# Kernel tuning notes

Measured on AMD Instinct MI355X. Metric: run time of the kernel, lower is better.

The kernel has to match this reference:

```python
import jax, jax.numpy as jnp
import numpy as np
import math

D_MODEL = 1024
D_HEAD = 64
BATCH = 8
SEQ = 2048


def setup_inputs() -> dict:
    key = jax.random.key(0)
    ks = jax.random.split(key, 5)
    s = 0.02
    return {
        "residual_stream": jax.random.normal(ks[0], (BATCH, SEQ, D_MODEL), dtype=jnp.float32),
        "Wq": jax.random.normal(ks[1], (D_HEAD, D_MODEL), dtype=jnp.float32) * s,
        "Wk": jax.random.normal(ks[2], (D_HEAD, D_MODEL), dtype=jnp.float32) * s,
        "Wv": jax.random.normal(ks[3], (D_HEAD, D_MODEL), dtype=jnp.float32) * s,
        "Wo": jax.random.normal(ks[4], (D_MODEL, D_HEAD), dtype=jnp.float32) * s,
    }


def reference(residual_stream, Wq, Wk, Wv, Wo):
    # NOTE: module scales by 1/sqrt(d_model), NOT 1/sqrt(d_head)
    scale = 1.0 / math.sqrt(D_MODEL)
    q = jnp.einsum('bsd,hd->bsh', residual_stream, Wq)  # [B,S,Dh]
    k = jnp.einsum('bsd,hd->bsh', residual_stream, Wk)  # [B,S,Dh]
    scores = jnp.einsum('bqh,bkh->bqk', q, k) * scale   # [B,S,S]
    seq = scores.shape[-1]
    causal = jnp.tril(jnp.ones((seq, seq), dtype=bool))
    scores = jnp.where(causal[None, :, :], scores, jnp.float32(-jnp.inf))
    attn = jax.nn.softmax(scores, axis=-1)
    # O applied to V *before* the attention-weighted sum (as in the module)
    x = jnp.einsum('bsh,dh->bsd', jnp.einsum('bsd,hd->bsh', residual_stream, Wv), Wo)  # [B,S,Dm]
    return jnp.einsum('bqk,bkd->bqd', attn, x)
```

## Files before the change

kernel.cpp:

```cpp
#include <hip/hip_runtime.h>

#define SEQ 2048
#define DMODEL 1024
#define DHEAD 64
#define NROWS 16384
#define ATT_SCALE 0.03125f

typedef __attribute__((ext_vector_type(8))) short bf16x8;
typedef __attribute__((ext_vector_type(4))) float f32x4;
typedef __attribute__((ext_vector_type(4))) unsigned int u32x4;
typedef __attribute__((ext_vector_type(4))) unsigned short u16x4;
typedef __attribute__((ext_vector_type(4))) float fl4;

#define MFMA16(a,b,c) __builtin_amdgcn_mfma_f32_16x16x32_bf16((a),(b),(c),0,0,0)
#define GLL16(g, l) __builtin_amdgcn_global_load_lds( \
    (const __attribute__((address_space(1))) void*)(g), \
    (__attribute__((address_space(3))) void*)(l), 16, 0, 0)

__device__ __forceinline__ unsigned short f2bf(float f) {
    union { float f; unsigned int u; } v; v.f = f;
    unsigned int u = v.u;
    unsigned int r = u + 0x7fffu + ((u >> 16) & 1u);
    return (unsigned short)(r >> 16);
}

__global__ __launch_bounds__(256) void k_cvt(
    const float* __restrict__ Wq, const float* __restrict__ Wk,
    const float* __restrict__ Wv, const float* __restrict__ Wo,
    unsigned short* __restrict__ Wb,
    unsigned short* __restrict__ Wob)
{
    int i4 = blockIdx.x * 256 + threadIdx.x;
    const int W1 = 16384;
    const float* src; unsigned short* dst; int off;
    if (i4 < 3 * W1) {
        int which = i4 / W1;
        off = i4 - which * W1;
        src = (which == 0) ? Wq : (which == 1) ? Wk : Wv;
        dst = Wb + (size_t)which * 65536;
    } else {
        off = i4 - 3 * W1; src = Wo; dst = Wob;
    }
    fl4 v = reinterpret_cast<const fl4*>(src)[off];
    u16x4 o;
    o[0] = f2bf(v[0]); o[1] = f2bf(v[1]); o[2] = f2bf(v[2]); o[3] = f2bf(v[3]);
    reinterpret_cast<u16x4*>(dst)[off] = o;
}

__global__ __launch_bounds__(256) void k_qkv(
    const float* __restrict__ x,
    const unsigned short* __restrict__ Wb,
    unsigned short* __restrict__ Qb,
    unsigned short* __restrict__ Kb,
    unsigned short* __restrict__ Vt)
{
    __shared__ __align__(16) char smem[81920];

    int tid = threadIdx.x;
    int wave = tid >> 6, lane = tid & 63, g = lane >> 4, lr = lane & 15;
    int mbase = blockIdx.x * 64;

    const float* xsrc[4];
#pragma unroll
    for (int j = 0; j < 4; ++j) {
        int ci = (wave * 4 + j) * 64 + lane;
        int row = ci >> 4, c = ci & 15, cg = c ^ (row & 7);
        xsrc[j] = x + (size_t)(mbase + row) * DMODEL + cg * 4;
    }
    const unsigned short* wsrc[6];
#pragma unroll
    for (int j = 0; j < 6; ++j) {
        int ci = (wave * 6 + j) * 64 + lane;
        int row = ci >> 3, c = ci & 7, cg = c ^ (row & 7);
        wsrc[j] = Wb + (size_t)row * DMODEL + cg * 8;
    }

    f32x4 acc[12];
#pragma unroll
    for (int f = 0; f < 12; ++f) acc[f] = (f32x4){0.f, 0.f, 0.f, 0.f};

#pragma unroll
    for (int j = 0; j < 4; ++j) GLL16(xsrc[j], smem + (wave * 4 + j) * 1024);
#pragma unroll
    for (int j = 0; j < 6; ++j) GLL16(wsrc[j], smem + 32768 + (wave * 6 + j) * 1024);

    for (int ks = 0; ks < 16; ++ks) {
        int cur = ks & 1;
        if (ks < 15) {
            int nb = cur ^ 1;
#pragma unroll
            for (int j = 0; j < 4; ++j)
                GLL16(xsrc[j] + (ks + 1) * 64, smem + nb * 16384 + (wave * 4 + j) * 1024);
#pragma unroll
            for (int j = 0; j < 6; ++j)
                GLL16(wsrc[j] + (ks + 1) * 64, smem + 32768 + nb * 24576 + (wave * 6 + j) * 1024);
            asm volatile("s_waitcnt vmcnt(10)" ::: "memory");
        } else {
            asm volatile("s_waitcnt vmcnt(0)" ::: "memory");
        }
        __builtin_amdgcn_s_barrier();
        asm volatile("" ::: "memory");

        const float* Xf = (const float*)(smem + cur * 16384);
        const unsigned short* Wf = (const unsigned short*)(smem + 32768 + cur * 24576);
        int arow = wave * 16 + lr;
#pragma unroll
        for (int kc = 0; kc < 2; ++kc) {
            int c0 = (kc * 8 + g * 2) ^ (lr & 7);
            int c1 = (kc * 8 + g * 2 + 1) ^ (lr & 7);
            fl4 xa = *(const fl4*)&Xf[arow * 64 + c0 * 4];
            fl4 xb = *(const fl4*)&Xf[arow * 64 + c1 * 4];
            bf16x8 a;
            a[0] = (short)f2bf(xa[0]); a[1] = (short)f2bf(xa[1]);
            a[2] = (short)f2bf(xa[2]); a[3] = (short)f2bf(xa[3]);
            a[4] = (short)f2bf(xb[0]); a[5] = (short)f2bf(xb[1]);
            a[6] = (short)f2bf(xb[2]); a[7] = (short)f2bf(xb[3]);
            __builtin_amdgcn_s_setprio(1);
#pragma unroll
            for (int f = 0; f < 12; ++f) {
                int brow = f * 16 + lr;
                int cb = (kc * 4 + g) ^ (lr & 7);
                bf16x8 b = *(const bf16x8*)&Wf[brow * 64 + cb * 8];
                acc[f] = MFMA16(a, b, acc[f]);
            }
            __builtin_amdgcn_s_setprio(0);
        }
        asm volatile("" ::: "memory");
        __builtin_amdgcn_s_barrier();
    }

    int mrow = mbase + wave * 16 + g * 4;
#pragma unroll
    for (int f = 0; f < 8; ++f) {
        int col = f * 16 + lr;
#pragma unroll
        for (int r = 0; r < 4; ++r) {
            unsigned short bv = f2bf(acc[f][r]);
            if (f < 4) Qb[(size_t)(mrow + r) * DHEAD + col] = bv;
            else       Kb[(size_t)(mrow + r) * DHEAD + col - 64] = bv;
        }
    }
    unsigned short* tmp = (unsigned short*)smem;
#pragma unroll
    for (int f = 8; f < 12; ++f) {
        int h = (f - 8) * 16 + lr;
#pragma unroll
        for (int r = 0; r < 4; ++r)
            tmp[(wave * 16 + g * 4 + r) * 72 + h] = f2bf(acc[f][r]);
    }
    __syncthreads();
    int b = mbase >> 11, sbase = mbase & 2047;
    int h = tid >> 2, sc = tid & 3;
    u32x4 o0, o1;
#pragma unroll
    for (int j = 0; j < 4; ++j) {
        o0[j] = (unsigned int)tmp[(sc * 16 + 2 * j) * 72 + h] |
                ((unsigned int)tmp[(sc * 16 + 2 * j + 1) * 72 + h] << 16);
        o1[j] = (unsigned int)tmp[(sc * 16 + 8 + 2 * j) * 72 + h] |
                ((unsigned int)tmp[(sc * 16 + 9 + 2 * j) * 72 + h] << 16);
    }
    size_t off = ((size_t)(b * 64 + h)) * SEQ + sbase + sc * 16;
    *reinterpret_cast<u32x4*>(&Vt[off]) = o0;
    *reinterpret_cast<u32x4*>(&Vt[off + 8]) = o1;
}

__global__ __launch_bounds__(128) void k_attn(
    const unsigned short* __restrict__ Qb,
    const unsigned short* __restrict__ Kb,
    const unsigned short* __restrict__ Vt,
    float* __restrict__ Op,
    float* __restrict__ Lp)
{
    __shared__ __align__(16) char smem[36864];

    int tid = threadIdx.x;
    int wave = tid >> 6, lane = tid & 63, g = lane >> 4, lr = lane & 15;
    int bid = blockIdx.x;
    int qt = 63 - (bid >> 4);
    int sub = bid & 15;
    int b = sub >> 1, chunk = sub & 1;
    int nt = qt / 2 + 1;
    int my_nt = (nt + 1 - chunk) >> 1;
    int qg = qt * 32 + wave * 16;
    size_t qrowbase = (size_t)(b * SEQ) + qg;

    bf16x8 aq[2];
#pragma unroll
    for (int kc = 0; kc < 2; ++kc)
        aq[kc] = *reinterpret_cast<const bf16x8*>(
            &Qb[(qrowbase + lr) * DHEAD + kc * 32 + g * 8]);

    const unsigned short* ksrc[4];
    const unsigned short* vsrc[4];
#pragma unroll
    for (int j = 0; j < 4; ++j) {
        int ci = wave * 256 + j * 64 + lane;
        int row = ci >> 3, c = ci & 7, cg = c ^ (row & 7);
        ksrc[j] = Kb + ((size_t)(b * SEQ) + row) * DHEAD + cg * 8;
        vsrc[j] = Vt + ((size_t)(b * DHEAD) + row) * SEQ + cg * 8;
    }

    float l_part[4];
    f32x4 of[4];
#pragma unroll
    for (int r = 0; r < 4; ++r) l_part[r] = 0.f;
#pragma unroll
    for (int f = 0; f < 4; ++f) of[f] = (f32x4){0.f, 0.f, 0.f, 0.f};

    if (my_nt > 0) {
#pragma unroll
        for (int j = 0; j < 4; ++j)
            GLL16(ksrc[j] + (size_t)chunk * 64 * DHEAD, smem + wave * 4096 + j * 1024);
#pragma unroll
        for (int j = 0; j < 4; ++j)
            GLL16(vsrc[j] + chunk * 64, smem + 16384 + wave * 4096 + j * 1024);

        for (int i = 0; i < my_nt; ++i) {
            int t = chunk + 2 * i;
            int cur = i & 1;
            if (i + 1 < my_nt) {
                int nb = cur ^ 1;
#pragma unroll
                for (int j = 0; j < 4; ++j)
                    GLL16(ksrc[j] + (size_t)(t + 2) * 64 * DHEAD,
                          smem + nb * 8192 + wave * 4096 + j * 1024);
#pragma unroll
                for (int j = 0; j < 4; ++j)
                    GLL16(vsrc[j] + (t + 2) * 64,
                          smem + 16384 + nb * 8192 + wave * 4096 + j * 1024);
                asm volatile("s_waitcnt vmcnt(8)" ::: "memory");
            } else {
                asm volatile("s_waitcnt vmcnt(0)" ::: "memory");
            }
            __builtin_amdgcn_s_barrier();
            asm volatile("" ::: "memory");

            const unsigned short* Kl = (const unsigned short*)(smem + cur * 8192);
            const unsigned short* Vl = (const unsigned short*)(smem + 16384 + cur * 8192);
            unsigned short* Pl = (unsigned short*)(smem + 32768) + wave * 1024;
            int kvb = t * 64;

            f32x4 s[4];
#pragma unroll
            for (int f = 0; f < 4; ++f) s[f] = (f32x4){0.f, 0.f, 0.f, 0.f};
            __builtin_amdgcn_s_setprio(1);
#pragma unroll
            for (int kc = 0; kc < 2; ++kc) {
#pragma unroll
                for (int f = 0; f < 4; ++f) {
                    int brow = f * 16 + lr;
                    int cb = (kc * 4 + g) ^ (lr & 7);
                    bf16x8 bk = *(const bf16x8*)&Kl[brow * 64 + cb * 8];
                    s[f] = MFMA16(aq[kc], bk, s[f]);
                }
            }
            __builtin_amdgcn_s_setprio(0);

#pragma unroll
            for (int f = 0; f < 4; ++f) {
                int kvg = kvb + f * 16 + lr;
#pragma unroll
                for (int r = 0; r < 4; ++r) {
                    int qr = qg + g * 4 + r;
                    float p = (kvg > qr) ? 0.f : __expf(s[f][r] * ATT_SCALE);
                    s[f][r] = p;
                    l_part[r] += p;
                }
            }
#pragma unroll
            for (int f = 0; f < 4; ++f) {
#pragma unroll
                for (int r = 0; r < 4; ++r) {
                    int row = g * 4 + r, col = f * 16 + lr;
                    int ch = (col >> 3) ^ (row & 7);
                    Pl[row * 64 + ch * 8 + (col & 7)] = f2bf(s[f][r]);
                }
            }
#pragma unroll
            for (int kc = 0; kc < 2; ++kc) {
                int cp = (kc * 4 + g) ^ (lr & 7);
                bf16x8 ap = *(const bf16x8*)&Pl[lr * 64 + cp * 8];
                __builtin_amdgcn_s_setprio(1);
#pragma unroll
                for (int fd = 0; fd < 4; ++fd) {
                    int vrow = fd * 16 + lr;
                    int cv = (kc * 4 + g) ^ (lr & 7);
                    bf16x8 bv = *(const bf16x8*)&Vl[vrow * 64 + cv * 8];
                    of[fd] = MFMA16(ap, bv, of[fd]);
                }
                __builtin_amdgcn_s_setprio(0);
            }
            asm volatile("" ::: "memory");
            __builtin_amdgcn_s_barrier();
        }
    }

    float* opb = Op + ((size_t)chunk * NROWS + qrowbase) * 64;
#pragma unroll
    for (int r = 0; r < 4; ++r) {
        float ls = l_part[r];
        ls += __shfl_xor(ls, 1); ls += __shfl_xor(ls, 2);
        ls += __shfl_xor(ls, 4); ls += __shfl_xor(ls, 8);
        if (lr == 0)
            Lp[(size_t)chunk * NROWS + qrowbase + g * 4 + r] = ls;
#pragma unroll
        for (int fd = 0; fd < 4; ++fd)
            opb[(g * 4 + r) * 64 + fd * 16 + lr] = of[fd][r];
    }
}

__global__ __launch_bounds__(256) void k_oproj(
    const float* __restrict__ Op,
    const float* __restrict__ Lp,
    const unsigned short* __restrict__ Wob,
    float* __restrict__ out)
{
    __shared__ __align__(16) unsigned short Wl[256 * 64];
    int tid = threadIdx.x;
    int wave = tid >> 6, lane = tid & 63, g = lane >> 4, lr = lane & 15;
    int mb = blockIdx.x * 64, nb = blockIdx.y * 256;

#pragma unroll
    for (int p = 0; p < 8; ++p) {
        int idx = p * 256 + tid;
        int row = idx >> 3, c = idx & 7;
        int ch = c ^ (row & 7);
        u32x4 v = *reinterpret_cast<const u32x4*>(
            &Wob[(size_t)(nb + row) * DHEAD + c * 8]);
        *reinterpret_cast<u32x4*>(&Wl[row * 64 + ch * 8]) = v;
    }
    __syncthreads();

    int row = mb + wave * 16 + lr;
    float inv = 1.0f / (Lp[row] + Lp[NROWS + row]);
    bf16x8 ao[2];
#pragma unroll
    for (int kc = 0; kc < 2; ++kc) {
        const float* p0 = &Op[(size_t)row * 64 + kc * 32 + g * 8];
        const float* p1 = &Op[(size_t)(NROWS + row) * 64 + kc * 32 + g * 8];
        fl4 a0 = *(const fl4*)p0, b0 = *(const fl4*)(p0 + 4);
        fl4 a1 = *(const fl4*)p1, b1 = *(const fl4*)(p1 + 4);
#pragma unroll
        for (int j = 0; j < 4; ++j) {
            ao[kc][j]     = (short)f2bf((a0[j] + a1[j]) * inv);
            ao[kc][j + 4] = (short)f2bf((b0[j] + b1[j]) * inv);
        }
    }

    f32x4 acc[16];
#pragma unroll
    for (int f = 0; f < 16; ++f) acc[f] = (f32x4){0.f, 0.f, 0.f, 0.f};
#pragma unroll
    for (int kc = 0; kc < 2; ++kc) {
        __builtin_amdgcn_s_setprio(1);
#pragma unroll
        for (int f = 0; f < 16; ++f) {
            int brow = f * 16 + lr;
            int cb = (kc * 4 + g) ^ (brow & 7);
            bf16x8 bw = *reinterpret_cast<const bf16x8*>(&Wl[brow * 64 + cb * 8]);
            acc[f] = MFMA16(ao[kc], bw, acc[f]);
        }
        __builtin_amdgcn_s_setprio(0);
    }
    int mrow = mb + wave * 16 + g * 4;
#pragma unroll
    for (int f = 0; f < 16; ++f) {
#pragma unroll
        for (int r = 0; r < 4; ++r)
            out[(size_t)(mrow + r) * DMODEL + nb + f * 16 + lr] = acc[f][r];
    }
}

extern "C" void kernel_launch(void* const* d_in, const int* in_sizes, int n_in,
                              void* d_out, int out_size, void* d_ws, size_t ws_size,
                              hipStream_t stream) {
    const float* x  = (const float*)d_in[0];
    const float* Wq = (const float*)d_in[1];
    const float* Wk = (const float*)d_in[2];
    const float* Wv = (const float*)d_in[3];
    const float* Wo = (const float*)d_in[4];
    float* out = (float*)d_out;

    unsigned short* Wb  = (unsigned short*)d_ws;
    unsigned short* Wob = Wb + 196608;
    unsigned short* Qb  = Wob + 65536;
    unsigned short* Kb  = Qb + 1048576;
    unsigned short* Vt  = Kb + 1048576;
    float* Op = (float*)(Vt + 1048576);
    float* Lp = Op + 2 * NROWS * 64;

    k_cvt<<<256, 256, 0, stream>>>(Wq, Wk, Wv, Wo, Wb, Wob);
    k_qkv<<<256, 256, 0, stream>>>(x, Wb, Qb, Kb, Vt);
    k_attn<<<1024, 128, 0, stream>>>(Qb, Kb, Vt, Op, Lp);
    k_oproj<<<dim3(256, 4), 256, 0, stream>>>(Op, Lp, Wob, out);
}
```

Baseline: 68.05 us.

## Enlarge attention query tiles, skip masked KV tiles, use packed bf16 conversion

The attention kernel now runs 4 waves per block over 64 query rows instead of 2 waves over 32. Each K/V tile loaded into shared memory is therefore reused by twice as many query rows, and the grid is halved. Waves whose rows lie entirely above a KV tile skip its compute, and fully unmasked tiles drop the mask test. The exp is rewritten as exp2 with a prescaled constant. Separately, fp32-to-bf16 packing in the QKV and output-projection kernels uses the hardware v_cvt_pk_bf16_f32 instruction instead of software rounding. The risk is wave divergence at the barriers and lower occupancy from the larger blocks.

```diff
diff --git a/kernel.cpp b/kernel.cpp
--- a/kernel.cpp
+++ b/kernel.cpp
@@ -4,7 +4,7 @@
 #define DMODEL 1024
 #define DHEAD 64
 #define NROWS 16384
-#define ATT_SCALE 0.03125f
+#define ATT_SC2 0.0450842300667f
 
 typedef __attribute__((ext_vector_type(8))) short bf16x8;
 typedef __attribute__((ext_vector_type(4))) float f32x4;
@@ -22,6 +22,12 @@
     unsigned int u = v.u;
     unsigned int r = u + 0x7fffu + ((u >> 16) & 1u);
     return (unsigned short)(r >> 16);
+}
+
+__device__ __forceinline__ unsigned int cvtpk(float lo, float hi) {
+    unsigned int d;
+    asm volatile("v_cvt_pk_bf16_f32 %0, %1, %2" : "=v"(d) : "v"(lo), "v"(hi));
+    return d;
 }
 
 __global__ __launch_bounds__(256) void k_cvt(
@@ -110,18 +116,16 @@
             int c1 = (kc * 8 + g * 2 + 1) ^ (lr & 7);
             fl4 xa = *(const fl4*)&Xf[arow * 64 + c0 * 4];
             fl4 xb = *(const fl4*)&Xf[arow * 64 + c1 * 4];
-            bf16x8 a;
-            a[0] = (short)f2bf(xa[0]); a[1] = (short)f2bf(xa[1]);
-            a[2] = (short)f2bf(xa[2]); a[3] = (short)f2bf(xa[3]);
-            a[4] = (short)f2bf(xb[0]); a[5] = (short)f2bf(xb[1]);
-            a[6] = (short)f2bf(xb[2]); a[7] = (short)f2bf(xb[3]);
+            union { unsigned int u[4]; bf16x8 v; } a;
+            a.u[0] = cvtpk(xa[0], xa[1]); a.u[1] = cvtpk(xa[2], xa[3]);
+            a.u[2] = cvtpk(xb[0], xb[1]); a.u[3] = cvtpk(xb[2], xb[3]);
             __builtin_amdgcn_s_setprio(1);
 #pragma unroll
             for (int f = 0; f < 12; ++f) {
                 int brow = f * 16 + lr;
                 int cb = (kc * 4 + g) ^ (lr & 7);
                 bf16x8 b = *(const bf16x8*)&Wf[brow * 64 + cb * 8];
-                acc[f] = MFMA16(a, b, acc[f]);
+                acc[f] = MFMA16(a.v, b, acc[f]);
             }
             __builtin_amdgcn_s_setprio(0);
         }
@@ -164,25 +168,25 @@
     *reinterpret_cast<u32x4*>(&Vt[off + 8]) = o1;
 }
 
-__global__ __launch_bounds__(128) void k_attn(
+__global__ __launch_bounds__(256) void k_attn(
     const unsigned short* __restrict__ Qb,
     const unsigned short* __restrict__ Kb,
     const unsigned short* __restrict__ Vt,
     float* __restrict__ Op,
     float* __restrict__ Lp)
 {
-    __shared__ __align__(16) char smem[36864];
+    __shared__ __align__(16) char smem[40960];
 
     int tid = threadIdx.x;
     int wave = tid >> 6, lane = tid & 63, g = lane >> 4, lr = lane & 15;
     int bid = blockIdx.x;
-    int qt = 63 - (bid >> 4);
+    int qt = 31 - (bid >> 4);
     int sub = bid & 15;
     int b = sub >> 1, chunk = sub & 1;
-    int nt = qt / 2 + 1;
+    int nt = qt + 1;
     int my_nt = (nt + 1 - chunk) >> 1;
-    int qg = qt * 32 + wave * 16;
-    size_t qrowbase = (size_t)(b * SEQ) + qg;
+    int qw = qt * 64 + wave * 16;
+    size_t qrowbase = (size_t)(b * SEQ) + qw;
 
     bf16x8 aq[2];
 #pragma unroll
@@ -190,11 +194,11 @@
         aq[kc] = *reinterpret_cast<const bf16x8*>(
             &Qb[(qrowbase + lr) * DHEAD + kc * 32 + g * 8]);
 
-    const unsigned short* ksrc[4];
-    const unsigned short* vsrc[4];
-#pragma unroll
-    for (int j = 0; j < 4; ++j) {
-        int ci = wave * 256 + j * 64 + lane;
+    const unsigned short* ksrc[2];
+    const unsigned short* vsrc[2];
+#pragma unroll
+    for (int j = 0; j < 2; ++j) {
+        int ci = j * 256 + tid;
         int row = ci >> 3, c = ci & 7, cg = c ^ (row & 7);
         ksrc[j] = Kb + ((size_t)(b * SEQ) + row) * DHEAD + cg * 8;
         vsrc[j] = Vt + ((size_t)(b * DHEAD) + row) * SEQ + cg * 8;
@@ -209,86 +213,100 @@
 
     if (my_nt > 0) {
 #pragma unroll
-        for (int j = 0; j < 4; ++j)
-            GLL16(ksrc[j] + (size_t)chunk * 64 * DHEAD, smem + wave * 4096 + j * 1024);
-#pragma unroll
-        for (int j = 0; j < 4; ++j)
-            GLL16(vsrc[j] + chunk * 64, smem + 16384 + wave * 4096 + j * 1024);
+        for (int j = 0; j < 2; ++j)
+            GLL16(ksrc[j] + (size_t)chunk * 64 * DHEAD, smem + j * 4096 + wave * 1024);
+#pragma unroll
+        for (int j = 0; j < 2; ++j)
+            GLL16(vsrc[j] + chunk * 64, smem + 16384 + j * 4096 + wave * 1024);
 
         for (int i = 0; i < my_nt; ++i) {
             int t = chunk + 2 * i;
             int cur = i & 1;
+            int kvb = t * 64;
             if (i + 1 < my_nt) {
                 int nb = cur ^ 1;
 #pragma unroll
-                for (int j = 0; j < 4; ++j)
+                for (int j = 0; j < 2; ++j)
                     GLL16(ksrc[j] + (size_t)(t + 2) * 64 * DHEAD,
-                          smem + nb * 8192 + wave * 4096 + j * 1024);
-#pragma unroll
-                for (int j = 0; j < 4; ++j)
+                          smem + nb * 8192 + j * 4096 + wave * 1024);
+#pragma unroll
+                for (int j = 0; j < 2; ++j)
                     GLL16(vsrc[j] + (t + 2) * 64,
-                          smem + 16384 + nb * 8192 + wave * 4096 + j * 1024);
-                asm volatile("s_waitcnt vmcnt(8)" ::: "memory");
+                          smem + 16384 + nb * 8192 + j * 4096 + wave * 1024);
+                asm volatile("s_waitcnt vmcnt(4)" ::: "memory");
             } else {
                 asm volatile("s_waitcnt vmcnt(0)" ::: "memory");
             }
             __builtin_amdgcn_s_barrier();
             asm volatile("" ::: "memory");
 
-            const unsigned short* Kl = (const unsigned short*)(smem + cur * 8192);
-            const unsigned short* Vl = (const unsigned short*)(smem + 16384 + cur * 8192);
-            unsigned short* Pl = (unsigned short*)(smem + 32768) + wave * 1024;
-            int kvb = t * 64;
-
-            f32x4 s[4];
-#pragma unroll
-            for (int f = 0; f < 4; ++f) s[f] = (f32x4){0.f, 0.f, 0.f, 0.f};
-            __builtin_amdgcn_s_setprio(1);
-#pragma unroll
-            for (int kc = 0; kc < 2; ++kc) {
-#pragma unroll
-                for (int f = 0; f < 4; ++f) {
-                    int brow = f * 16 + lr;
-                    int cb = (kc * 4 + g) ^ (lr & 7);
-                    bf16x8 bk = *(const bf16x8*)&Kl[brow * 64 + cb * 8];
-                    s[f] = MFMA16(aq[kc], bk, s[f]);
-                }
-            }
-            __builtin_amdgcn_s_setprio(0);
-
-#pragma unroll
-            for (int f = 0; f < 4; ++f) {
-                int kvg = kvb + f * 16 + lr;
-#pragma unroll
-                for (int r = 0; r < 4; ++r) {
-                    int qr = qg + g * 4 + r;
-                    float p = (kvg > qr) ? 0.f : __expf(s[f][r] * ATT_SCALE);
-                    s[f][r] = p;
-                    l_part[r] += p;
-                }
-            }
-#pragma unroll
-            for (int f = 0; f < 4; ++f) {
-#pragma unroll
-                for (int r = 0; r < 4; ++r) {
-                    int row = g * 4 + r, col = f * 16 + lr;
-                    int ch = (col >> 3) ^ (row & 7);
-                    Pl[row * 64 + ch * 8 + (col & 7)] = f2bf(s[f][r]);
-                }
-            }
-#pragma unroll
-            for (int kc = 0; kc < 2; ++kc) {
-                int cp = (kc * 4 + g) ^ (lr & 7);
-                bf16x8 ap = *(const bf16x8*)&Pl[lr * 64 + cp * 8];
+            if (kvb <= qw + 15) {
+                const unsigned short* Kl = (const unsigned short*)(smem + cur * 8192);
+                const unsigned short* Vl = (const unsigned short*)(smem + 16384 + cur * 8192);
+                unsigned short* Pl = (unsigned short*)(smem + 32768) + wave * 1024;
+
+                f32x4 s[4];
+#pragma unroll
+                for (int f = 0; f < 4; ++f) s[f] = (f32x4){0.f, 0.f, 0.f, 0.f};
                 __builtin_amdgcn_s_setprio(1);
 #pragma unroll
-                for (int fd = 0; fd < 4; ++fd) {
-                    int vrow = fd * 16 + lr;
-                    int cv = (kc * 4 + g) ^ (lr & 7);
-                    bf16x8 bv = *(const bf16x8*)&Vl[vrow * 64 + cv * 8];
-                    of[fd] = MFMA16(ap, bv, of[fd]);
+                for (int kc = 0; kc < 2; ++kc) {
+#pragma unroll
+                    for (int f = 0; f < 4; ++f) {
+                        int brow = f * 16 + lr;
+                        int cb = (kc * 4 + g) ^ (lr & 7);
+                        bf16x8 bk = *(const bf16x8*)&Kl[brow * 64 + cb * 8];
+                        s[f] = MFMA16(aq[kc], bk, s[f]);
+                    }
                 }
                 __builtin_amdgcn_s_setprio(0);
+
+                if (kvb + 63 <= qw) {
+#pragma unroll
+                    for (int f = 0; f < 4; ++f)
+#pragma unroll
+                        for (int r = 0; r < 4; ++r) {
+                            float p = exp2f(s[f][r] * ATT_SC2);
+                            s[f][r] = p;
+                            l_part[r] += p;
+                        }
+                } else {
+#pragma unroll
+                    for (int f = 0; f < 4; ++f) {
+                        int kvg = kvb + f * 16 + lr;
+#pragma unroll
+                        for (int r = 0; r < 4; ++r) {
+                            int qr = qw + g * 4 + r;
+                            float p = exp2f(s[f][r] * ATT_SC2);
+                            p = (kvg > qr) ? 0.f : p;
+                            s[f][r] = p;
+                            l_part[r] += p;
+                        }
+                    }
+                }
+#pragma unroll
+                for (int f = 0; f < 4; ++f) {
+#pragma unroll
+                    for (int r = 0; r < 4; ++r) {
+                        int row = g * 4 + r, col = f * 16 + lr;
+                        int ch = (col >> 3) ^ (row & 7);
+                        Pl[row * 64 + ch * 8 + (col & 7)] = f2bf(s[f][r]);
+                    }
+                }
+#pragma unroll
+                for (int kc = 0; kc < 2; ++kc) {
+                    int cp = (kc * 4 + g) ^ (lr & 7);
+                    bf16x8 ap = *(const bf16x8*)&Pl[lr * 64 + cp * 8];
+                    __builtin_amdgcn_s_setprio(1);
+#pragma unroll
+                    for (int fd = 0; fd < 4; ++fd) {
+                        int vrow = fd * 16 + lr;
+                        int cv = (kc * 4 + g) ^ (lr & 7);
+                        bf16x8 bv = *(const bf16x8*)&Vl[vrow * 64 + cv * 8];
+                        of[fd] = MFMA16(ap, bv, of[fd]);
+                    }
+                    __builtin_amdgcn_s_setprio(0);
+                }
             }
             asm volatile("" ::: "memory");
             __builtin_amdgcn_s_barrier();
@@ -340,11 +358,12 @@
         const float* p1 = &Op[(size_t)(NROWS + row) * 64 + kc * 32 + g * 8];
         fl4 a0 = *(const fl4*)p0, b0 = *(const fl4*)(p0 + 4);
         fl4 a1 = *(const fl4*)p1, b1 = *(const fl4*)(p1 + 4);
-#pragma unroll
-        for (int j = 0; j < 4; ++j) {
-            ao[kc][j]     = (short)f2bf((a0[j] + a1[j]) * inv);
-            ao[kc][j + 4] = (short)f2bf((b0[j] + b1[j]) * inv);
-        }
+        union { unsigned int u[4]; bf16x8 v; } a;
+        a.u[0] = cvtpk((a0[0] + a1[0]) * inv, (a0[1] + a1[1]) * inv);
+        a.u[1] = cvtpk((a0[2] + a1[2]) * inv, (a0[3] + a1[3]) * inv);
+        a.u[2] = cvtpk((b0[0] + b1[0]) * inv, (b0[1] + b1[1]) * inv);
+        a.u[3] = cvtpk((b0[2] + b1[2]) * inv, (b0[3] + b1[3]) * inv);
+        ao[kc] = a.v;
     }
 
     f32x4 acc[16];
@@ -391,6 +410,6 @@
 
     k_cvt<<<256, 256, 0, stream>>>(Wq, Wk, Wv, Wo, Wb, Wob);
     k_qkv<<<256, 256, 0, stream>>>(x, Wb, Qb, Kb, Vt);
-    k_attn<<<1024, 128, 0, stream>>>(Qb, Kb, Vt, Op, Lp);
+    k_attn<<<512, 256, 0, stream>>>(Qb, Kb, Vt, Op, Lp);
     k_oproj<<<dim3(256, 4), 256, 0, stream>>>(Op, Lp, Wob, out);
 }
```

New measurement: 66.47 us. 2.3% less time.
